# Kernel tuning notes

Measured on AMD Instinct MI355X. Metric: run time of the kernel, lower is better.

The kernel has to match this reference:

```python
import jax, jax.numpy as jnp
import numpy as np

D_MODEL = 1024
NUM_HEADS = 16
D_K = D_MODEL // NUM_HEADS


def setup_inputs() -> dict:
    key = jax.random.key(0)
    ks = jax.random.split(key, 9)
    s = 1.0 / np.sqrt(D_MODEL)
    inp = {
        "x": jax.random.normal(ks[0], (2, 2048, D_MODEL), dtype=jnp.float32),
        "Wq": jax.random.uniform(ks[1], (D_MODEL, D_MODEL), jnp.float32, -s, s),
        "bq": jax.random.uniform(ks[2], (D_MODEL,), jnp.float32, -s, s),
        "Wk": jax.random.uniform(ks[3], (D_MODEL, D_MODEL), jnp.float32, -s, s),
        "bk": jax.random.uniform(ks[4], (D_MODEL,), jnp.float32, -s, s),
        "Wv": jax.random.uniform(ks[5], (D_MODEL, D_MODEL), jnp.float32, -s, s),
        "bv": jax.random.uniform(ks[6], (D_MODEL,), jnp.float32, -s, s),
        "Wo": jax.random.uniform(ks[7], (D_MODEL, D_MODEL), jnp.float32, -s, s),
        "bo": jax.random.uniform(ks[8], (D_MODEL,), jnp.float32, -s, s),
    }
    return inp


def reference(x, Wq, bq, Wk, bk, Wv, bv, Wo, bo):
    B, S, _ = x.shape
    # projections (torch Linear: y = x @ W.T + b)
    q = x @ Wq.T + bq
    k = x @ Wk.T + bk
    v = x @ Wv.T + bv
    # [B, H, S, Dk]
    q = q.reshape(B, S, NUM_HEADS, D_K).transpose(0, 2, 1, 3)
    k = k.reshape(B, S, NUM_HEADS, D_K).transpose(0, 2, 1, 3)
    v = v.reshape(B, S, NUM_HEADS, D_K).transpose(0, 2, 1, 3)
    scale = 1.0 / np.sqrt(D_K).astype(np.float32)
    energy = jnp.einsum("bhqd,bhkd->bhqk", q, k) * scale
    attn = jax.nn.softmax(energy, axis=-1)
    out = jnp.einsum("bhqk,bhkd->bhqd", attn, v)
    out = out.transpose(0, 2, 1, 3).reshape(B, S, D_MODEL)
    return out @ Wo.T + bo
```

## Files before the change

kernel.cpp:

```cpp
#include <hip/hip_runtime.h>
#include <hip/hip_bf16.h>
#include <cstdint>

typedef __bf16 bf16;
typedef __bf16 bf16x4 __attribute__((ext_vector_type(4)));
typedef __bf16 bf16x8 __attribute__((ext_vector_type(8)));
typedef float f32x4 __attribute__((ext_vector_type(4)));
typedef float f32x16 __attribute__((ext_vector_type(16)));
typedef unsigned int u32x4 __attribute__((ext_vector_type(4)));

#define DM   1024
#define SEQ  2048
#define NH   16
#define DKH  64

__device__ __forceinline__ bf16x8 ld8(const bf16* p) {
    return *reinterpret_cast<const bf16x8*>(p);
}

__device__ __forceinline__ void gld16(const void* g, void* lds) {
    __builtin_amdgcn_global_load_lds(
        (__attribute__((address_space(1))) void*)(uintptr_t)g,
        (__attribute__((address_space(3))) void*)(uint32_t)(uintptr_t)lds,
        16, 0, 0);
}

__device__ __forceinline__ f32x4 mfma16(bf16x8 a, bf16x8 b, f32x4 c) {
    return __builtin_amdgcn_mfma_f32_16x16x32_bf16(a, b, c, 0, 0, 0);
}
__device__ __forceinline__ f32x16 mfma32(bf16x8 a, bf16x8 b, f32x16 c) {
    return __builtin_amdgcn_mfma_f32_32x32x16_bf16(a, b, c, 0, 0, 0);
}

__device__ __forceinline__ unsigned pkbf(float lo, float hi) {
    unsigned r;
    asm("v_cvt_pk_bf16_f32 %0, %1, %2" : "=v"(r) : "v"(lo), "v"(hi));
    return r;
}
__device__ __forceinline__ void plswap(unsigned& a, unsigned& b) {
    asm volatile("v_permlane32_swap_b32 %0, %1" : "+v"(a), "+v"(b));
}

__global__ __launch_bounds__(256) void cvt_all(
    const float4* __restrict__ x,  const float4* __restrict__ wq,
    const float4* __restrict__ wk, const float4* __restrict__ wv,
    const float4* __restrict__ wo,
    ushort4* __restrict__ xb,  ushort4* __restrict__ wqb,
    ushort4* __restrict__ wkb, ushort4* __restrict__ wvb,
    ushort4* __restrict__ wob) {
    int i = blockIdx.x * 256 + threadIdx.x;
    const float4* src;
    ushort4* dst;
    int off;
    if (i < 1048576) {
        src = x; dst = xb; off = i;
    } else {
        int r = i - 1048576;
        int sel = r >> 18;
        off = r & 262143;
        src = sel == 0 ? wq : sel == 1 ? wk : sel == 2 ? wv : wo;
        dst = sel == 0 ? wqb : sel == 1 ? wkb : sel == 2 ? wvb : wob;
    }
    float4 f = src[off];
    ushort4 u;
    u.x = __builtin_bit_cast(unsigned short, (bf16)f.x);
    u.y = __builtin_bit_cast(unsigned short, (bf16)f.y);
    u.z = __builtin_bit_cast(unsigned short, (bf16)f.z);
    u.w = __builtin_bit_cast(unsigned short, (bf16)f.w);
    dst[off] = u;
}

template <int OUT_MODE>
__device__ __forceinline__ void gemm_body(const bf16* __restrict__ A,
                                          const bf16* __restrict__ W,
                                          const float* __restrict__ bias,
                                          void* __restrict__ outp,
                                          int m0, int n0, float scale,
                                          bf16* __restrict__ S) {
    constexpr int BK = 32;
    const int t    = threadIdx.x;
    const int lane = t & 63;
    const int r16  = lane & 15, grp = lane >> 4;
    const int wave = t >> 6;
    const int wr   = (wave >> 1) * 64;
    const int wc   = (wave & 1) * 64;

    f32x4 acc[4][4] = {};

    const int srow = t >> 2;
    const int scol = t & 3;

    auto STAGE = [&](int buf, int kt) {
#pragma unroll
        for (int i = 0; i < 2; ++i) {
            const int row = i * 64 + srow;
            const int cs = (scol ^ (row & 3)) * 8;
            gld16(A + (size_t)(m0 + row) * DM + kt * BK + cs,
                  &S[buf * 8192 + i * 2048 + t * 8]);
            gld16(W + (size_t)(n0 + row) * DM + kt * BK + cs,
                  &S[buf * 8192 + 4096 + i * 2048 + t * 8]);
        }
    };

    STAGE(0, 0);
    STAGE(1, 1);

#pragma unroll
    for (int kt = 0; kt < 32; ++kt) {
        if (kt == 31) { asm volatile("s_waitcnt vmcnt(0)" ::: "memory"); }
        else          { asm volatile("s_waitcnt vmcnt(4)" ::: "memory"); }
        __builtin_amdgcn_sched_barrier(0);
        __builtin_amdgcn_s_barrier();
        __builtin_amdgcn_sched_barrier(0);

        if (kt < 30) STAGE((kt + 2) % 3, kt + 2);

        const bf16* Ab = &S[(kt % 3) * 8192];
        const bf16* Bb = Ab + 4096;
        bf16x8 af[4], bfr[4];
#pragma unroll
        for (int m = 0; m < 4; ++m) {
            const int row = wr + m * 16 + r16;
            af[m] = ld8(&Ab[row * BK + ((grp ^ (row & 3)) * 8)]);
        }
#pragma unroll
        for (int n = 0; n < 4; ++n) {
            const int row = wc + n * 16 + r16;
            bfr[n] = ld8(&Bb[row * BK + ((grp ^ (row & 3)) * 8)]);
        }
        __builtin_amdgcn_s_setprio(1);
#pragma unroll
        for (int m = 0; m < 4; ++m)
#pragma unroll
            for (int n = 0; n < 4; ++n)
                acc[m][n] = mfma16(af[m], bfr[n], acc[m][n]);
        __builtin_amdgcn_s_setprio(0);
    }

    if constexpr (OUT_MODE == 2) {
        __syncthreads();
        bf16* Tw = &S[wave * 4096];
        const int b = m0 >> 11;
        const int tokbase = (m0 & 2047) + wr;
#pragma unroll
        for (int n = 0; n < 4; ++n) {
            const int dim = n * 16 + r16;
            const float bvv = bias[n0 - 2048 + wc + dim];
#pragma unroll
            for (int m = 0; m < 4; ++m) {
                bf16x4 w4 = {(bf16)(acc[m][n][0] + bvv), (bf16)(acc[m][n][1] + bvv),
                             (bf16)(acc[m][n][2] + bvv), (bf16)(acc[m][n][3] + bvv)};
                const int slot = (m * 2 + (grp >> 1)) ^ (dim & 7);
                *reinterpret_cast<bf16x4*>(&Tw[dim * 64 + slot * 8 + (grp & 1) * 4]) = w4;
            }
        }
        asm volatile("" ::: "memory");
#pragma unroll
        for (int r = 0; r < 8; ++r) {
            const int dim = (lane >> 3) + 8 * r;
            const int ts  = lane & 7;
            bf16x8 v = ld8(&Tw[dim * 64 + ((ts ^ (dim & 7)) * 8)]);
            const int col = n0 - 2048 + wc + dim;
            bf16* dst = (bf16*)outp +
                ((size_t)(b * NH + (col >> 6)) * DKH + (col & 63)) * SEQ +
                tokbase + ts * 8;
            *reinterpret_cast<bf16x8*>(dst) = v;
        }
    } else {
#pragma unroll
        for (int n = 0; n < 4; ++n) {
            const int col = (OUT_MODE == 0 ? (n0 & 1023) : n0) + wc + n * 16 + r16;
            const float bvv = bias[col];
#pragma unroll
            for (int m = 0; m < 4; ++m) {
                const int row = m0 + wr + m * 16 + grp * 4;
#pragma unroll
                for (int j = 0; j < 4; ++j) {
                    float v = (acc[m][n][j] + bvv) * scale;
                    if constexpr (OUT_MODE == 1)
                        ((float*)outp)[(size_t)(row + j) * DM + col] = v;
                    else
                        ((bf16*)outp)[(size_t)(row + j) * DM + col] = (bf16)v;
                }
            }
        }
    }
}

__global__ __launch_bounds__(256, 3) void gemm_qkv(
    const bf16* __restrict__ xb, const bf16* __restrict__ wqkv,
    const float* __restrict__ bq, const float* __restrict__ bk,
    const float* __restrict__ bv_,
    bf16* __restrict__ q, bf16* __restrict__ k, bf16* __restrict__ vt) {
    __shared__ __attribute__((aligned(16))) bf16 S[24576];
    int id = blockIdx.x;
    id = (id & 7) * 96 + (id >> 3);
    const int nt = id % 24, mt = id / 24;
    const int m0 = mt * 128, n0 = nt * 128;
    if (nt < 8) {
        gemm_body<0>(xb, wqkv, bq, q, m0, n0, 0.18033688f, S);
    } else if (nt < 16) {
        gemm_body<0>(xb, wqkv, bk, k, m0, n0, 1.0f, S);
    } else {
        gemm_body<2>(xb, wqkv, bv_, vt, m0, n0, 1.0f, S);
    }
}

__global__ __launch_bounds__(256, 3) void gemm_out(
    const bf16* __restrict__ ab, const bf16* __restrict__ wob,
    const float* __restrict__ bo, float* __restrict__ out) {
    __shared__ __attribute__((aligned(16))) bf16 S[24576];
    int id = blockIdx.x;
    id = (id & 7) * 32 + (id >> 3);
    const int m0 = (id >> 3) * 128, n0 = (id & 7) * 128;
    gemm_body<1>(ab, wob, bo, out, m0, n0, 1.0f, S);
}

__global__ __launch_bounds__(256, 2) void attn(const bf16* __restrict__ Q,
                                               const bf16* __restrict__ K,
                                               const bf16* __restrict__ VT,
                                               bf16* __restrict__ O) {
    __shared__ __attribute__((aligned(16))) bf16 S[2][2][8192];

    const int t = threadIdx.x, lane = t & 63, wave = t >> 6;
    const int l31 = lane & 31, hi = lane >> 5;
    const int kvh = wave >> 1;
    const int qw  = wave & 1;

    int id = blockIdx.x;
    id = (id & 7) * 64 + (id >> 3);
    const int qt = id & 15, h = (id >> 4) & 15, b = id >> 8;

    const bf16* Qb = Q + ((size_t)b * SEQ + qt * 128) * DM + h * DKH;
    const bf16* Kb = K + (size_t)b * SEQ * DM + h * DKH;
    const bf16* Vb = VT + (size_t)((b * NH + h) * DKH) * SEQ;

    bf16x8 qf[2][4];
#pragma unroll
    for (int u = 0; u < 2; ++u)
#pragma unroll
        for (int c = 0; c < 4; ++c)
            qf[u][c] = ld8(Qb + (size_t)(qw * 64 + u * 32 + l31) * DM + c * 16 + hi * 8);

    const bf16 one = (bf16)1.0f;
    const bf16x8 ones8 = {one, one, one, one, one, one, one, one};

    f32x16 o[2][2] = {};
    f32x16 ol[2] = {};

    const int sr = t >> 3, scs = t & 7;

    auto STAGE = [&](int buf, int step) {
#pragma unroll
        for (int hf = 0; hf < 2; ++hf) {
            const int kt = hf * 1024 + step * 64;
            bf16* Kd = &S[hf][buf][0];
            bf16* Vd = &S[hf][buf][4096];
#pragma unroll
            for (int i = 0; i < 2; ++i) {
                const int r = i * 32 + sr;
                const int cs = (scs ^ (r & 7)) * 8;
                gld16(Kb + (size_t)(kt + r) * DM + cs, Kd + i * 2048 + t * 8);
                gld16(Vb + (size_t)r * SEQ + kt + cs, Vd + i * 2048 + t * 8);
            }
        }
    };

    auto TILE = [&](const bf16* KsB, const bf16* VsB) {
        u32x4 up[2][4];
#pragma unroll
        for (int sub = 0; sub < 2; ++sub) {
            const int krow = sub * 32 + l31;
            const int ksw  = krow & 7;
            bf16x8 kf[4];
#pragma unroll
            for (int c = 0; c < 4; ++c)
                kf[c] = ld8(&KsB[krow * 64 + (((c * 2 + hi) ^ ksw) * 8)]);
            f32x16 ss0 = {}, ss1 = {};
            __builtin_amdgcn_s_setprio(1);
#pragma unroll
            for (int c = 0; c < 4; ++c) ss0 = mfma32(kf[c], qf[0][c], ss0);
#pragma unroll
            for (int c = 0; c < 4; ++c) ss1 = mfma32(kf[c], qf[1][c], ss1);
            __builtin_amdgcn_s_setprio(0);
#pragma unroll
            for (int u = 0; u < 2; ++u) {
                const f32x16& ss = u ? ss1 : ss0;
                float e[16];
#pragma unroll
                for (int r = 0; r < 16; ++r)
                    e[r] = __builtin_amdgcn_exp2f(ss[r]);
                unsigned u0 = pkbf(e[0],  e[1]),  u1 = pkbf(e[2],  e[3]);
                unsigned u2 = pkbf(e[4],  e[5]),  u3 = pkbf(e[6],  e[7]);
                unsigned u4 = pkbf(e[8],  e[9]),  u5 = pkbf(e[10], e[11]);
                unsigned u6 = pkbf(e[12], e[13]), u7 = pkbf(e[14], e[15]);
                plswap(u0, u2); plswap(u1, u3);
                plswap(u4, u6); plswap(u5, u7);
                up[u][sub * 2]     = u32x4{u0, u1, u2, u3};
                up[u][sub * 2 + 1] = u32x4{u4, u5, u6, u7};
            }
        }

        __builtin_amdgcn_s_setprio(1);
#pragma unroll
        for (int dt = 0; dt < 2; ++dt) {
            const int vrow = dt * 32 + l31;
            const int vsw  = vrow & 7;
#pragma unroll
            for (int kc = 0; kc < 4; ++kc) {
                const bf16x8 vf = ld8(&VsB[vrow * 64 + (((kc * 2 + hi) ^ vsw) * 8)]);
                o[0][dt] = mfma32(__builtin_bit_cast(bf16x8, up[0][kc]), vf, o[0][dt]);
                o[1][dt] = mfma32(__builtin_bit_cast(bf16x8, up[1][kc]), vf, o[1][dt]);
            }
        }
#pragma unroll
        for (int kc = 0; kc < 4; ++kc) {
            ol[0] = mfma32(__builtin_bit_cast(bf16x8, up[0][kc]), ones8, ol[0]);
            ol[1] = mfma32(__builtin_bit_cast(bf16x8, up[1][kc]), ones8, ol[1]);
        }
        __builtin_amdgcn_s_setprio(0);
    };

#define GATE(N) do {                                              \
        asm volatile("s_waitcnt vmcnt(" #N ")" ::: "memory");     \
        __builtin_amdgcn_sched_barrier(0);                        \
    } while (0)
#define BAR() do {                                                \
        __builtin_amdgcn_sched_barrier(0);                        \
        __builtin_amdgcn_s_barrier();                             \
        __builtin_amdgcn_sched_barrier(0);                        \
    } while (0)

    STAGE(0, 0);
    STAGE(1, 1);

    GATE(8); TILE(&S[kvh][0][0], &S[kvh][0][4096]);
#pragma unroll 1
    for (int g = 0; g < 7; ++g) {
        BAR(); STAGE(0, 2 * g + 2);
        GATE(8); TILE(&S[kvh][1][0], &S[kvh][1][4096]);
        BAR(); STAGE(1, 2 * g + 3);
        GATE(8); TILE(&S[kvh][0][0], &S[kvh][0][4096]);
    }
    BAR();
    GATE(0); TILE(&S[kvh][1][0], &S[kvh][1][4096]);
#undef GATE
#undef BAR

    __syncthreads();
    float* Xs = (float*)&S[0][0][0];
    if (wave >= 2) {
        float* base = Xs + (wave - 2) * 6144;
#pragma unroll
        for (int u = 0; u < 2; ++u)
#pragma unroll
            for (int dt = 0; dt < 2; ++dt)
#pragma unroll
                for (int g4 = 0; g4 < 4; ++g4) {
                    f32x4 v = {o[u][dt][g4 * 4], o[u][dt][g4 * 4 + 1],
                               o[u][dt][g4 * 4 + 2], o[u][dt][g4 * 4 + 3]};
                    *reinterpret_cast<f32x4*>(
                        base + ((u * 2 + dt) * 4 + g4) * 256 + lane * 4) = v;
                }
#pragma unroll
        for (int u = 0; u < 2; ++u)
#pragma unroll
            for (int g4 = 0; g4 < 4; ++g4) {
                f32x4 v = {ol[u][g4 * 4], ol[u][g4 * 4 + 1],
                           ol[u][g4 * 4 + 2], ol[u][g4 * 4 + 3]};
                *reinterpret_cast<f32x4*>(
                    base + (16 + u * 4 + g4) * 256 + lane * 4) = v;
            }
    }
    __syncthreads();
    if (wave < 2) {
        const float* base = Xs + wave * 6144;
#pragma unroll
        for (int u = 0; u < 2; ++u)
#pragma unroll
            for (int dt = 0; dt < 2; ++dt)
#pragma unroll
                for (int g4 = 0; g4 < 4; ++g4) {
                    f32x4 v = *reinterpret_cast<const f32x4*>(
                        base + ((u * 2 + dt) * 4 + g4) * 256 + lane * 4);
#pragma unroll
                    for (int j = 0; j < 4; ++j) o[u][dt][g4 * 4 + j] += v[j];
                }
#pragma unroll
        for (int u = 0; u < 2; ++u)
#pragma unroll
            for (int g4 = 0; g4 < 4; ++g4) {
                f32x4 v = *reinterpret_cast<const f32x4*>(
                    base + (16 + u * 4 + g4) * 256 + lane * 4);
#pragma unroll
                for (int j = 0; j < 4; ++j) ol[u][g4 * 4 + j] += v[j];
            }

#pragma unroll
        for (int u = 0; u < 2; ++u) {
            float inv[16];
#pragma unroll
            for (int r = 0; r < 16; ++r) inv[r] = 1.0f / ol[u][r];
#pragma unroll
            for (int dt = 0; dt < 2; ++dt)
#pragma unroll
                for (int r = 0; r < 16; ++r) {
                    const int ql = (r & 3) + 8 * (r >> 2) + 4 * hi;
                    O[((size_t)b * SEQ + qt * 128 + qw * 64 + u * 32 + ql) * DM
                      + h * DKH + dt * 32 + l31] = (bf16)(o[u][dt][r] * inv[r]);
                }
        }
    }
}

extern "C" void kernel_launch(void* const* d_in, const int* in_sizes, int n_in,
                              void* d_out, int out_size, void* d_ws, size_t ws_size,
                              hipStream_t stream) {
    const float* x  = (const float*)d_in[0];
    const float* Wq = (const float*)d_in[1];
    const float* bq = (const float*)d_in[2];
    const float* Wk = (const float*)d_in[3];
    const float* bk = (const float*)d_in[4];
    const float* Wv = (const float*)d_in[5];
    const float* bv = (const float*)d_in[6];
    const float* Wo = (const float*)d_in[7];
    const float* bo = (const float*)d_in[8];
    float* out = (float*)d_out;

    char* ws = (char*)d_ws;
    bf16* xb   = (bf16*)(ws + 0);
    bf16* wqkv = (bf16*)(ws + 8388608);
    bf16* wqb  = (bf16*)(ws + 8388608);
    bf16* wkb  = (bf16*)(ws + 10485760);
    bf16* wvb  = (bf16*)(ws + 12582912);
    bf16* wob  = (bf16*)(ws + 14680064);
    bf16* qb   = (bf16*)(ws + 16777216);
    bf16* kb   = (bf16*)(ws + 25165824);
    bf16* ab   = (bf16*)(ws + 33554432);
    bf16* vtb  = (bf16*)(ws + 41943040);

    cvt_all<<<8192, 256, 0, stream>>>(
        (const float4*)x, (const float4*)Wq, (const float4*)Wk,
        (const float4*)Wv, (const float4*)Wo,
        (ushort4*)xb, (ushort4*)wqb, (ushort4*)wkb, (ushort4*)wvb, (ushort4*)wob);

    gemm_qkv<<<768, 256, 0, stream>>>(xb, wqkv, bq, bk, bv, qb, kb, vtb);

    attn<<<dim3(512), 256, 0, stream>>>(qb, kb, vtb, ab);

    gemm_out<<<256, 256, 0, stream>>>(ab, wob, bo, out);
}
```

Measured before the change: 105.4 us.

## Give each attention wave private KV staging buffers and compute row sums in registers

The attention kernel now gives each wave its own double-buffered 32-key K/V tile in LDS and loads it itself, so the block-wide barriers in the KV loop go away. Each wave's tile shrinks from 64 to 32 keys, and the loop runs 32 smaller tiles. The softmax denominator is now summed with plain adds on the exp values followed by cross-lane shuffles, replacing the extra MFMA against a ones vector. This removes synchronisation stalls and MFMA work, but each wave now issues more, smaller global-to-LDS loads with less reuse of K/V across the waves that share a KV half.

New measurement: 109.9 us. 4.3% more time.

```diff
diff --git a/kernel.cpp b/kernel.cpp
--- a/kernel.cpp
+++ b/kernel.cpp
@@ -220,7 +220,7 @@
                                                const bf16* __restrict__ K,
                                                const bf16* __restrict__ VT,
                                                bf16* __restrict__ O) {
-    __shared__ __attribute__((aligned(16))) bf16 S[2][2][8192];
+    __shared__ __attribute__((aligned(16))) bf16 S[4][2][4096];
 
     const int t = threadIdx.x, lane = t & 63, wave = t >> 6;
     const int l31 = lane & 31, hi = lane >> 5;
@@ -234,6 +234,7 @@
     const bf16* Qb = Q + ((size_t)b * SEQ + qt * 128) * DM + h * DKH;
     const bf16* Kb = K + (size_t)b * SEQ * DM + h * DKH;
     const bf16* Vb = VT + (size_t)((b * NH + h) * DKH) * SEQ;
+    const int kvbase = kvh << 10;
 
     bf16x8 qf[2][4];
 #pragma unroll
@@ -242,110 +243,102 @@
         for (int c = 0; c < 4; ++c)
             qf[u][c] = ld8(Qb + (size_t)(qw * 64 + u * 32 + l31) * DM + c * 16 + hi * 8);
 
-    const bf16 one = (bf16)1.0f;
-    const bf16x8 ones8 = {one, one, one, one, one, one, one, one};
-
     f32x16 o[2][2] = {};
-    f32x16 ol[2] = {};
-
-    const int sr = t >> 3, scs = t & 7;
-
-    auto STAGE = [&](int buf, int step) {
-#pragma unroll
-        for (int hf = 0; hf < 2; ++hf) {
-            const int kt = hf * 1024 + step * 64;
-            bf16* Kd = &S[hf][buf][0];
-            bf16* Vd = &S[hf][buf][4096];
-#pragma unroll
-            for (int i = 0; i < 2; ++i) {
-                const int r = i * 32 + sr;
-                const int cs = (scs ^ (r & 7)) * 8;
-                gld16(Kb + (size_t)(kt + r) * DM + cs, Kd + i * 2048 + t * 8);
-                gld16(Vb + (size_t)r * SEQ + kt + cs, Vd + i * 2048 + t * 8);
-            }
+    float Lp[2] = {0.f, 0.f};
+
+    bf16* W0 = &S[wave][0][0];
+    bf16* W1 = &S[wave][1][0];
+
+    auto STAGE = [&](bf16* dst, int tile) {
+        const int kt = kvbase + tile * 32;
+#pragma unroll
+        for (int i = 0; i < 4; ++i) {
+            const int r = i * 8 + (lane >> 3);
+            const int s = (lane & 7) ^ (r & 7);
+            gld16(Kb + (size_t)(kt + r) * DM + s * 8, dst + i * 512 + lane * 8);
+        }
+#pragma unroll
+        for (int i = 0; i < 4; ++i) {
+            const int d = i * 16 + (lane >> 2);
+            const int s = (lane & 3) ^ ((d >> 1) & 3);
+            gld16(Vb + (size_t)d * SEQ + kt + s * 8, dst + 2048 + i * 512 + lane * 8);
         }
     };
 
-    auto TILE = [&](const bf16* KsB, const bf16* VsB) {
-        u32x4 up[2][4];
-#pragma unroll
-        for (int sub = 0; sub < 2; ++sub) {
-            const int krow = sub * 32 + l31;
-            const int ksw  = krow & 7;
-            bf16x8 kf[4];
-#pragma unroll
-            for (int c = 0; c < 4; ++c)
-                kf[c] = ld8(&KsB[krow * 64 + (((c * 2 + hi) ^ ksw) * 8)]);
-            f32x16 ss0 = {}, ss1 = {};
-            __builtin_amdgcn_s_setprio(1);
-#pragma unroll
-            for (int c = 0; c < 4; ++c) ss0 = mfma32(kf[c], qf[0][c], ss0);
-#pragma unroll
-            for (int c = 0; c < 4; ++c) ss1 = mfma32(kf[c], qf[1][c], ss1);
-            __builtin_amdgcn_s_setprio(0);
-#pragma unroll
-            for (int u = 0; u < 2; ++u) {
-                const f32x16& ss = u ? ss1 : ss0;
-                float e[16];
-#pragma unroll
-                for (int r = 0; r < 16; ++r)
-                    e[r] = __builtin_amdgcn_exp2f(ss[r]);
-                unsigned u0 = pkbf(e[0],  e[1]),  u1 = pkbf(e[2],  e[3]);
-                unsigned u2 = pkbf(e[4],  e[5]),  u3 = pkbf(e[6],  e[7]);
-                unsigned u4 = pkbf(e[8],  e[9]),  u5 = pkbf(e[10], e[11]);
-                unsigned u6 = pkbf(e[12], e[13]), u7 = pkbf(e[14], e[15]);
-                plswap(u0, u2); plswap(u1, u3);
-                plswap(u4, u6); plswap(u5, u7);
-                up[u][sub * 2]     = u32x4{u0, u1, u2, u3};
-                up[u][sub * 2 + 1] = u32x4{u4, u5, u6, u7};
-            }
-        }
-
+    auto TILE = [&](const bf16* buf) {
+        const bf16* Kt = buf;
+        const bf16* Vt = buf + 2048;
+        bf16x8 kf[4];
+#pragma unroll
+        for (int c = 0; c < 4; ++c) {
+            const int slot = l31 * 8 + ((2 * c + hi) ^ (l31 & 7));
+            kf[c] = ld8(Kt + slot * 8);
+        }
+        f32x16 ss0 = {}, ss1 = {};
         __builtin_amdgcn_s_setprio(1);
 #pragma unroll
+        for (int c = 0; c < 4; ++c) ss0 = mfma32(kf[c], qf[0][c], ss0);
+#pragma unroll
+        for (int c = 0; c < 4; ++c) ss1 = mfma32(kf[c], qf[1][c], ss1);
+        __builtin_amdgcn_s_setprio(0);
+
+        u32x4 up[2][2];
+#pragma unroll
+        for (int u = 0; u < 2; ++u) {
+            const f32x16& ss = u ? ss1 : ss0;
+            float e[16];
+#pragma unroll
+            for (int r = 0; r < 16; ++r)
+                e[r] = __builtin_amdgcn_exp2f(ss[r]);
+            Lp[u] += ((e[0] + e[1]) + (e[2] + e[3])) + ((e[4] + e[5]) + (e[6] + e[7]))
+                   + ((e[8] + e[9]) + (e[10] + e[11])) + ((e[12] + e[13]) + (e[14] + e[15]));
+            unsigned u0 = pkbf(e[0],  e[1]),  u1 = pkbf(e[2],  e[3]);
+            unsigned u2 = pkbf(e[4],  e[5]),  u3 = pkbf(e[6],  e[7]);
+            unsigned u4 = pkbf(e[8],  e[9]),  u5 = pkbf(e[10], e[11]);
+            unsigned u6 = pkbf(e[12], e[13]), u7 = pkbf(e[14], e[15]);
+            plswap(u0, u2); plswap(u1, u3);
+            plswap(u4, u6); plswap(u5, u7);
+            up[u][0] = u32x4{u0, u1, u2, u3};
+            up[u][1] = u32x4{u4, u5, u6, u7};
+        }
+
+        __builtin_amdgcn_s_setprio(1);
+#pragma unroll
         for (int dt = 0; dt < 2; ++dt) {
-            const int vrow = dt * 32 + l31;
-            const int vsw  = vrow & 7;
-#pragma unroll
-            for (int kc = 0; kc < 4; ++kc) {
-                const bf16x8 vf = ld8(&VsB[vrow * 64 + (((kc * 2 + hi) ^ vsw) * 8)]);
+            const int d = dt * 32 + l31;
+#pragma unroll
+            for (int kc = 0; kc < 2; ++kc) {
+                const int slot = d * 4 + ((kc * 2 + hi) ^ ((d >> 1) & 3));
+                const bf16x8 vf = ld8(Vt + slot * 8);
                 o[0][dt] = mfma32(__builtin_bit_cast(bf16x8, up[0][kc]), vf, o[0][dt]);
                 o[1][dt] = mfma32(__builtin_bit_cast(bf16x8, up[1][kc]), vf, o[1][dt]);
             }
         }
-#pragma unroll
-        for (int kc = 0; kc < 4; ++kc) {
-            ol[0] = mfma32(__builtin_bit_cast(bf16x8, up[0][kc]), ones8, ol[0]);
-            ol[1] = mfma32(__builtin_bit_cast(bf16x8, up[1][kc]), ones8, ol[1]);
-        }
         __builtin_amdgcn_s_setprio(0);
     };
 
-#define GATE(N) do {                                              \
+#define GATEW(N) do {                                             \
         asm volatile("s_waitcnt vmcnt(" #N ")" ::: "memory");     \
         __builtin_amdgcn_sched_barrier(0);                        \
     } while (0)
-#define BAR() do {                                                \
-        __builtin_amdgcn_sched_barrier(0);                        \
-        __builtin_amdgcn_s_barrier();                             \
-        __builtin_amdgcn_sched_barrier(0);                        \
-    } while (0)
-
-    STAGE(0, 0);
-    STAGE(1, 1);
-
-    GATE(8); TILE(&S[kvh][0][0], &S[kvh][0][4096]);
+
+    STAGE(W0, 0);
+    STAGE(W1, 1);
+
 #pragma unroll 1
-    for (int g = 0; g < 7; ++g) {
-        BAR(); STAGE(0, 2 * g + 2);
-        GATE(8); TILE(&S[kvh][1][0], &S[kvh][1][4096]);
-        BAR(); STAGE(1, 2 * g + 3);
-        GATE(8); TILE(&S[kvh][0][0], &S[kvh][0][4096]);
-    }
-    BAR();
-    GATE(0); TILE(&S[kvh][1][0], &S[kvh][1][4096]);
-#undef GATE
-#undef BAR
+    for (int tt = 0; tt < 30; tt += 2) {
+        GATEW(8);
+        TILE(W0);
+        __builtin_amdgcn_sched_barrier(0);
+        STAGE(W0, tt + 2);
+        GATEW(8);
+        TILE(W1);
+        __builtin_amdgcn_sched_barrier(0);
+        if (tt + 3 < 32) STAGE(W1, tt + 3);
+    }
+    GATEW(8); TILE(W0);
+    GATEW(0); TILE(W1);
+#undef GATEW
 
     __syncthreads();
     float* Xs = (float*)&S[0][0][0];
@@ -362,15 +355,8 @@
                     *reinterpret_cast<f32x4*>(
                         base + ((u * 2 + dt) * 4 + g4) * 256 + lane * 4) = v;
                 }
-#pragma unroll
-        for (int u = 0; u < 2; ++u)
-#pragma unroll
-            for (int g4 = 0; g4 < 4; ++g4) {
-                f32x4 v = {ol[u][g4 * 4], ol[u][g4 * 4 + 1],
-                           ol[u][g4 * 4 + 2], ol[u][g4 * 4 + 3]};
-                *reinterpret_cast<f32x4*>(
-                    base + (16 + u * 4 + g4) * 256 + lane * 4) = v;
-            }
+        base[16 * 256 + lane] = Lp[0];
+        base[16 * 256 + 64 + lane] = Lp[1];
     }
     __syncthreads();
     if (wave < 2) {
@@ -386,28 +372,24 @@
 #pragma unroll
                     for (int j = 0; j < 4; ++j) o[u][dt][g4 * 4 + j] += v[j];
                 }
-#pragma unroll
-        for (int u = 0; u < 2; ++u)
-#pragma unroll
-            for (int g4 = 0; g4 < 4; ++g4) {
-                f32x4 v = *reinterpret_cast<const f32x4*>(
-                    base + (16 + u * 4 + g4) * 256 + lane * 4);
-#pragma unroll
-                for (int j = 0; j < 4; ++j) ol[u][g4 * 4 + j] += v[j];
-            }
+        Lp[0] += base[16 * 256 + lane];
+        Lp[1] += base[16 * 256 + 64 + lane];
 
 #pragma unroll
         for (int u = 0; u < 2; ++u) {
-            float inv[16];
-#pragma unroll
-            for (int r = 0; r < 16; ++r) inv[r] = 1.0f / ol[u][r];
+            const float Lf = Lp[u] + __shfl_xor(Lp[u], 32);
+            const float inv = 1.0f / Lf;
+            float invr[16];
+#pragma unroll
+            for (int r = 0; r < 16; ++r)
+                invr[r] = __shfl(inv, (r & 3) + 8 * (r >> 2) + 4 * hi);
 #pragma unroll
             for (int dt = 0; dt < 2; ++dt)
 #pragma unroll
                 for (int r = 0; r < 16; ++r) {
                     const int ql = (r & 3) + 8 * (r >> 2) + 4 * hi;
                     O[((size_t)b * SEQ + qt * 128 + qw * 64 + u * 32 + ql) * DM
-                      + h * DKH + dt * 32 + l31] = (bf16)(o[u][dt][r] * inv[r]);
+                      + h * DKH + dt * 32 + l31] = (bf16)(o[u][dt][r] * invr[r]);
                 }
         }
     }
```

## Rewrite QKV GEMM with 256x256 tiles, 8 waves, and quarter-phased staging pipeline

Applied to the files above, without the earlier changes.

Replaces the QKV projection GEMM's 128x128 tile, 4-wave kernel with a 256x256 tile, 512-thread kernel using BK=64. The K loop is split into four phases per k-tile, with async global-to-LDS loads interleaved and gated by explicit vmcnt waits and barriers. The goal is more data reuse per LDS load and more overlap of memory with MFMA work. In exchange it launches only 192 blocks, which is fewer than the number of CUs, so some compute units sit idle. It also uses about 136KB of LDS and allows one block per CU. gemm_out is inlined and left functionally unchanged.

Measured after the change: 103.0 us. 2.2% less time.

```diff
diff --git a/kernel.cpp b/kernel.cpp
--- a/kernel.cpp
+++ b/kernel.cpp
@@ -70,25 +70,174 @@
     dst[off] = u;
 }
 
-template <int OUT_MODE>
-__device__ __forceinline__ void gemm_body(const bf16* __restrict__ A,
-                                          const bf16* __restrict__ W,
-                                          const float* __restrict__ bias,
-                                          void* __restrict__ outp,
-                                          int m0, int n0, float scale,
-                                          bf16* __restrict__ S) {
+__global__ __launch_bounds__(512, 1) void gemm_qkv(
+    const bf16* __restrict__ xb, const bf16* __restrict__ wqkv,
+    const float* __restrict__ bq, const float* __restrict__ bk,
+    const float* __restrict__ bv_,
+    bf16* __restrict__ q_, bf16* __restrict__ k_, bf16* __restrict__ vt) {
+    __shared__ __attribute__((aligned(16))) bf16 S[69632];
+
+    const int t = threadIdx.x, lane = t & 63;
+    const int r16 = lane & 15, grp = lane >> 4;
+    const int wave = t >> 6;
+    const int wr = (wave >> 2) * 128;
+    const int wc = (wave & 3) * 64;
+
+    int id = blockIdx.x;
+    id = (id & 7) * 24 + (id >> 3);
+    const int nt = id % 12, mt = id / 12;
+    const int m0 = mt * 256, n0 = nt * 256;
+
+    f32x4 acc[8][4] = {};
+    const int srow = t >> 3, scol = t & 7;
+
+    auto STQ = [&](int dbuf, int tile, int which, int qq) {
+        const int row = qq * 64 + srow;
+        const int cs = (scol ^ (row & 7)) * 8;
+        const bf16* src = which
+            ? wqkv + (size_t)(n0 + row) * DM + tile * 64 + cs
+            : xb   + (size_t)(m0 + row) * DM + tile * 64 + cs;
+        gld16(src, &S[dbuf * 32768 + which * 16384 + qq * 4096 + t * 8]);
+    };
+
+    bf16x8 bfr[4][2];
+
+#define GATE(N) do {                                              \
+        asm volatile("s_waitcnt vmcnt(" #N ")" ::: "memory");     \
+        __builtin_amdgcn_sched_barrier(0);                        \
+        __builtin_amdgcn_s_barrier();                             \
+        __builtin_amdgcn_sched_barrier(0);                        \
+    } while (0)
+
+#define PHASE(d, q, stg, dostg) do {                                          \
+        if (dostg) {                                                          \
+            if ((q) == 0)      { STQ((d) ^ 1, stg, 1, 0); STQ((d) ^ 1, stg, 1, 1); } \
+            else if ((q) == 1) { STQ((d) ^ 1, stg, 1, 2); STQ((d) ^ 1, stg, 1, 3); } \
+            else if ((q) == 2) { STQ((d) ^ 1, stg, 0, 0); STQ((d) ^ 1, stg, 0, 2); } \
+            else               { STQ((d) ^ 1, stg, 0, 1); STQ((d) ^ 1, stg, 0, 3); } \
+        }                                                                     \
+        const bf16* Ab = &S[(d) * 32768];                                     \
+        const bf16* Bb = &S[(d) * 32768 + 16384];                             \
+        if ((q) == 0) {                                                       \
+            _Pragma("unroll")                                                 \
+            for (int n = 0; n < 4; ++n) {                                     \
+                const int row = wc + n * 16 + r16;                            \
+                bfr[n][0] = ld8(&Bb[row * 64 + ((grp ^ (row & 7)) * 8)]);     \
+                bfr[n][1] = ld8(&Bb[row * 64 + (((4 + grp) ^ (row & 7)) * 8)]); \
+            }                                                                 \
+        }                                                                     \
+        bf16x8 af0k0, af0k1, af1k0, af1k1;                                    \
+        { const int row = wr + ((q) * 2) * 16 + r16;                          \
+          af0k0 = ld8(&Ab[row * 64 + ((grp ^ (row & 7)) * 8)]);               \
+          af0k1 = ld8(&Ab[row * 64 + (((4 + grp) ^ (row & 7)) * 8)]); }       \
+        { const int row = wr + ((q) * 2 + 1) * 16 + r16;                      \
+          af1k0 = ld8(&Ab[row * 64 + ((grp ^ (row & 7)) * 8)]);               \
+          af1k1 = ld8(&Ab[row * 64 + (((4 + grp) ^ (row & 7)) * 8)]); }       \
+        __builtin_amdgcn_s_setprio(1);                                        \
+        _Pragma("unroll")                                                     \
+        for (int n = 0; n < 4; ++n) {                                         \
+            acc[(q) * 2][n]     = mfma16(af0k0, bfr[n][0], acc[(q) * 2][n]);  \
+            acc[(q) * 2][n]     = mfma16(af0k1, bfr[n][1], acc[(q) * 2][n]);  \
+            acc[(q) * 2 + 1][n] = mfma16(af1k0, bfr[n][0], acc[(q) * 2 + 1][n]); \
+            acc[(q) * 2 + 1][n] = mfma16(af1k1, bfr[n][1], acc[(q) * 2 + 1][n]); \
+        }                                                                     \
+        __builtin_amdgcn_s_setprio(0);                                        \
+    } while (0)
+
+    STQ(0, 0, 1, 0); STQ(0, 0, 1, 1); STQ(0, 0, 1, 2); STQ(0, 0, 1, 3);
+    STQ(0, 0, 0, 0); STQ(0, 0, 0, 2); STQ(0, 0, 0, 1); STQ(0, 0, 0, 3);
+
+#pragma unroll 1
+    for (int g = 0; g < 7; ++g) {
+        const int t0 = 2 * g;
+        GATE(2); PHASE(0, 0, t0 + 1, true);
+        GATE(4); PHASE(0, 1, t0 + 1, true);
+        GATE(4); PHASE(0, 2, t0 + 1, true);
+        GATE(6); PHASE(0, 3, t0 + 1, true);
+        GATE(2); PHASE(1, 0, t0 + 2, true);
+        GATE(4); PHASE(1, 1, t0 + 2, true);
+        GATE(4); PHASE(1, 2, t0 + 2, true);
+        GATE(6); PHASE(1, 3, t0 + 2, true);
+    }
+    GATE(2); PHASE(0, 0, 15, true);
+    GATE(4); PHASE(0, 1, 15, true);
+    GATE(4); PHASE(0, 2, 15, true);
+    GATE(6); PHASE(0, 3, 15, true);
+    GATE(2); PHASE(1, 0, 0, false);
+    GATE(2); PHASE(1, 1, 0, false);
+    GATE(0); PHASE(1, 2, 0, false);
+    GATE(0); PHASE(1, 3, 0, false);
+#undef GATE
+#undef PHASE
+
+    if (n0 < 2048) {
+        const float scale = (n0 < 1024) ? 0.18033688f : 1.0f;
+        bf16* out = (n0 < 1024) ? q_ : k_;
+        const float* bias = (n0 < 1024) ? bq : bk;
+        const int nc0 = n0 & 1023;
+#pragma unroll
+        for (int n = 0; n < 4; ++n) {
+            const int col = nc0 + wc + n * 16 + r16;
+            const float bvv = bias[col];
+#pragma unroll
+            for (int m = 0; m < 8; ++m) {
+                const int row = m0 + wr + m * 16 + grp * 4;
+#pragma unroll
+                for (int j = 0; j < 4; ++j)
+                    out[(size_t)(row + j) * DM + col] =
+                        (bf16)((acc[m][n][j] + bvv) * scale);
+            }
+        }
+    } else {
+        const int nc0 = n0 - 2048;
+        const int b = m0 >> 11;
+        const int s0 = (m0 & 2047) + wr;
+        __syncthreads();
+        bf16* Tw = &S[wave * 8704];
+#pragma unroll
+        for (int n = 0; n < 4; ++n) {
+            const int dl = n * 16 + r16;
+            const float bvv = bv_[nc0 + wc + dl];
+#pragma unroll
+            for (int m = 0; m < 8; ++m) {
+                bf16x4 w4 = {(bf16)(acc[m][n][0] + bvv), (bf16)(acc[m][n][1] + bvv),
+                             (bf16)(acc[m][n][2] + bvv), (bf16)(acc[m][n][3] + bvv)};
+                *reinterpret_cast<bf16x4*>(&Tw[dl * 136 + m * 16 + grp * 4]) = w4;
+            }
+        }
+        asm volatile("" ::: "memory");
+#pragma unroll
+        for (int dd = 0; dd < 8; ++dd) {
+            const int dim = dd * 8 + (lane >> 3);
+            const int col = nc0 + wc + dim;
+            bf16* dst = vt + ((size_t)(b * NH + (col >> 6)) * DKH + (col & 63)) * SEQ + s0;
+#pragma unroll
+            for (int cc = 0; cc < 2; ++cc) {
+                const int c = (lane & 7) + cc * 8;
+                bf16x8 v = ld8(&Tw[dim * 136 + c * 8]);
+                *reinterpret_cast<bf16x8*>(dst + c * 8) = v;
+            }
+        }
+    }
+}
+
+__global__ __launch_bounds__(256, 3) void gemm_out(
+    const bf16* __restrict__ A, const bf16* __restrict__ W,
+    const float* __restrict__ bias, float* __restrict__ out) {
     constexpr int BK = 32;
+    __shared__ __attribute__((aligned(16))) bf16 S[24576];
     const int t    = threadIdx.x;
     const int lane = t & 63;
     const int r16  = lane & 15, grp = lane >> 4;
     const int wave = t >> 6;
     const int wr   = (wave >> 1) * 64;
     const int wc   = (wave & 1) * 64;
+    int id = blockIdx.x;
+    id = (id & 7) * 32 + (id >> 3);
+    const int m0 = (id >> 3) * 128, n0 = (id & 7) * 128;
 
     f32x4 acc[4][4] = {};
-
-    const int srow = t >> 2;
-    const int scol = t & 3;
+    const int srow = t >> 2, scol = t & 3;
 
     auto STAGE = [&](int buf, int kt) {
 #pragma unroll
@@ -137,83 +286,18 @@
         __builtin_amdgcn_s_setprio(0);
     }
 
-    if constexpr (OUT_MODE == 2) {
-        __syncthreads();
-        bf16* Tw = &S[wave * 4096];
-        const int b = m0 >> 11;
-        const int tokbase = (m0 & 2047) + wr;
-#pragma unroll
-        for (int n = 0; n < 4; ++n) {
-            const int dim = n * 16 + r16;
-            const float bvv = bias[n0 - 2048 + wc + dim];
-#pragma unroll
-            for (int m = 0; m < 4; ++m) {
-                bf16x4 w4 = {(bf16)(acc[m][n][0] + bvv), (bf16)(acc[m][n][1] + bvv),
-                             (bf16)(acc[m][n][2] + bvv), (bf16)(acc[m][n][3] + bvv)};
-                const int slot = (m * 2 + (grp >> 1)) ^ (dim & 7);
-                *reinterpret_cast<bf16x4*>(&Tw[dim * 64 + slot * 8 + (grp & 1) * 4]) = w4;
-            }
-        }
-        asm volatile("" ::: "memory");
-#pragma unroll
-        for (int r = 0; r < 8; ++r) {
-            const int dim = (lane >> 3) + 8 * r;
-            const int ts  = lane & 7;
-            bf16x8 v = ld8(&Tw[dim * 64 + ((ts ^ (dim & 7)) * 8)]);
-            const int col = n0 - 2048 + wc + dim;
-            bf16* dst = (bf16*)outp +
-                ((size_t)(b * NH + (col >> 6)) * DKH + (col & 63)) * SEQ +
-                tokbase + ts * 8;
-            *reinterpret_cast<bf16x8*>(dst) = v;
-        }
-    } else {
-#pragma unroll
-        for (int n = 0; n < 4; ++n) {
-            const int col = (OUT_MODE == 0 ? (n0 & 1023) : n0) + wc + n * 16 + r16;
-            const float bvv = bias[col];
-#pragma unroll
-            for (int m = 0; m < 4; ++m) {
-                const int row = m0 + wr + m * 16 + grp * 4;
-#pragma unroll
-                for (int j = 0; j < 4; ++j) {
-                    float v = (acc[m][n][j] + bvv) * scale;
-                    if constexpr (OUT_MODE == 1)
-                        ((float*)outp)[(size_t)(row + j) * DM + col] = v;
-                    else
-                        ((bf16*)outp)[(size_t)(row + j) * DM + col] = (bf16)v;
-                }
-            }
-        }
-    }
-}
-
-__global__ __launch_bounds__(256, 3) void gemm_qkv(
-    const bf16* __restrict__ xb, const bf16* __restrict__ wqkv,
-    const float* __restrict__ bq, const float* __restrict__ bk,
-    const float* __restrict__ bv_,
-    bf16* __restrict__ q, bf16* __restrict__ k, bf16* __restrict__ vt) {
-    __shared__ __attribute__((aligned(16))) bf16 S[24576];
-    int id = blockIdx.x;
-    id = (id & 7) * 96 + (id >> 3);
-    const int nt = id % 24, mt = id / 24;
-    const int m0 = mt * 128, n0 = nt * 128;
-    if (nt < 8) {
-        gemm_body<0>(xb, wqkv, bq, q, m0, n0, 0.18033688f, S);
-    } else if (nt < 16) {
-        gemm_body<0>(xb, wqkv, bk, k, m0, n0, 1.0f, S);
-    } else {
-        gemm_body<2>(xb, wqkv, bv_, vt, m0, n0, 1.0f, S);
-    }
-}
-
-__global__ __launch_bounds__(256, 3) void gemm_out(
-    const bf16* __restrict__ ab, const bf16* __restrict__ wob,
-    const float* __restrict__ bo, float* __restrict__ out) {
-    __shared__ __attribute__((aligned(16))) bf16 S[24576];
-    int id = blockIdx.x;
-    id = (id & 7) * 32 + (id >> 3);
-    const int m0 = (id >> 3) * 128, n0 = (id & 7) * 128;
-    gemm_body<1>(ab, wob, bo, out, m0, n0, 1.0f, S);
+#pragma unroll
+    for (int n = 0; n < 4; ++n) {
+        const int col = n0 + wc + n * 16 + r16;
+        const float bvv = bias[col];
+#pragma unroll
+        for (int m = 0; m < 4; ++m) {
+            const int row = m0 + wr + m * 16 + grp * 4;
+#pragma unroll
+            for (int j = 0; j < 4; ++j)
+                out[(size_t)(row + j) * DM + col] = acc[m][n][j] + bvv;
+        }
+    }
 }
 
 __global__ __launch_bounds__(256, 2) void attn(const bf16* __restrict__ Q,
@@ -444,7 +528,7 @@
         (const float4*)Wv, (const float4*)Wo,
         (ushort4*)xb, (ushort4*)wqb, (ushort4*)wkb, (ushort4*)wvb, (ushort4*)wob);
 
-    gemm_qkv<<<768, 256, 0, stream>>>(xb, wqkv, bq, bk, bv, qb, kb, vtb);
+    gemm_qkv<<<192, 512, 0, stream>>>(xb, wqkv, bq, bk, bv, qb, kb, vtb);
 
     attn<<<dim3(512), 256, 0, stream>>>(qb, kb, vtb, ab);
 
```
